# Kernel optimization log

Hardware: AMD Instinct MI355X
Metric: run time of the kernel (lower is better)

## Reference

```python
import jax, jax.numpy as jnp
import numpy as np

R, C, B, E, H = 128, 256, 1, 768, 12
DK = E // H

def setup_inputs() -> dict:
    key = jax.random.key(0)
    ks = jax.random.split(key, 5)
    s = 1.0 / np.sqrt(E)
    return {
        "x": jax.random.normal(ks[0], (R, C, B, E), jnp.float32),
        "Wq": jax.random.normal(ks[1], (E, E), jnp.float32) * s,
        "bq": jnp.zeros((E,), jnp.float32),
        "Wk": jax.random.normal(ks[2], (E, E), jnp.float32) * s,
        "bk": jnp.zeros((E,), jnp.float32),
        "Wv": jax.random.normal(ks[3], (E, E), jnp.float32) * s,
        "bv": jnp.zeros((E,), jnp.float32),
        "Wo": jax.random.normal(ks[4], (E, E), jnp.float32) * s,
        "bo": jnp.zeros((E,), jnp.float32),
    }

def reference(x, Wq, bq, Wk, bk, Wv, bv, Wo, bo):
    n_rows, n_cols, batch, emb = x.shape
    scaling = (DK ** -0.5) / jnp.sqrt(jnp.float32(n_rows))
    # projections (torch Linear: x @ W.T + b)
    q = (x @ Wq.T + bq).reshape(n_rows, n_cols, batch, H, DK) * scaling
    k = (x @ Wk.T + bk).reshape(n_rows, n_cols, batch, H, DK)
    v = (x @ Wv.T + bv).reshape(n_rows, n_cols, batch, H, DK)
    # pooled attention logits: sum over rows r -> [H, B, C, C]
    attn = jnp.einsum('rinhd,rjnhd->hnij', q, k)
    probs = jax.nn.softmax(attn, axis=-1)  # single softmax shared across rows
    # context: [R, C, B, H, DK]
    c = jnp.einsum('hnij,rjnhd->rinhd', probs, v).reshape(n_rows, n_cols, batch, emb)
    out = c @ Wo.T + bo
    return out, probs
```

## Files before the change

kernel.cpp:

```cpp
#include <hip/hip_runtime.h>
#include <math.h>

#define R_  128
#define C_  256
#define E_  768
#define H_  12
#define DK_ 64
#define T_  (R_*C_)
#define RS_ 8
#define LP  40

typedef __attribute__((ext_vector_type(8))) short          bf16x8;
typedef __attribute__((ext_vector_type(4))) float          f32x4;
typedef __attribute__((ext_vector_type(4))) unsigned short u16x4;
typedef __attribute__((ext_vector_type(8))) unsigned short u16x8;

struct HL { unsigned short h, l; };

__device__ __forceinline__ HL split2(float f) {
    HL o;
    unsigned int u = __float_as_uint(f);
    o.h = (unsigned short)(u >> 16);
    float r = f - __uint_as_float(u & 0xFFFF0000u);
    o.l = (unsigned short)(__float_as_uint(r) >> 16);
    return o;
}

template<int AMODE, int OMODE>
__global__ __launch_bounds__(256, 2) void gemm_kernel(
    const float* __restrict__ A32,
    const unsigned short* __restrict__ Ah, const unsigned short* __restrict__ Al,
    const float* __restrict__ B32, const float* __restrict__ bias, float scale,
    float* __restrict__ Y32, unsigned short* __restrict__ Yh, unsigned short* __restrict__ Yl)
{
    __shared__ __align__(16) unsigned short smem[20480];
    unsigned short* AsH = smem;
    unsigned short* AsL = smem + 5120;
    unsigned short* BsH = smem + 10240;
    unsigned short* BsL = smem + 15360;

    const int tid  = threadIdx.x;
    const int m0   = blockIdx.x * 128;
    const int n0   = blockIdx.y * 128;
    const int wave = tid >> 6, lane = tid & 63;
    const int wm   = (wave & 1) * 64, wn = (wave >> 1) * 64;
    const int fr   = lane & 15;
    const int kq   = (lane >> 4) * 8;
    const int srow = tid >> 1;
    const int sk   = (tid & 1) * 16;

    f32x4 acc[4][4] = {};

    for (int k0 = 0; k0 < E_; k0 += 32) {
        if constexpr (AMODE == 0) {
            const float* ap = A32 + (size_t)(m0 + srow) * E_ + k0 + sk;
            #pragma unroll
            for (int c = 0; c < 4; ++c) {
                float4 f = *(const float4*)(ap + 4 * c);
                u16x4 h4, l4;
                HL e0 = split2(f.x), e1 = split2(f.y), e2 = split2(f.z), e3 = split2(f.w);
                h4[0] = e0.h; h4[1] = e1.h; h4[2] = e2.h; h4[3] = e3.h;
                l4[0] = e0.l; l4[1] = e1.l; l4[2] = e2.l; l4[3] = e3.l;
                *(u16x4*)&AsH[srow * LP + sk + 4 * c] = h4;
                *(u16x4*)&AsL[srow * LP + sk + 4 * c] = l4;
            }
        } else {
            const unsigned short* aph = Ah + (size_t)(m0 + srow) * E_ + k0 + sk;
            const unsigned short* apl = Al + (size_t)(m0 + srow) * E_ + k0 + sk;
            *(u16x8*)&AsH[srow * LP + sk]     = *(const u16x8*)aph;
            *(u16x8*)&AsH[srow * LP + sk + 8] = *(const u16x8*)(aph + 8);
            *(u16x8*)&AsL[srow * LP + sk]     = *(const u16x8*)apl;
            *(u16x8*)&AsL[srow * LP + sk + 8] = *(const u16x8*)(apl + 8);
        }
        {
            const float* bp = B32 + (size_t)(n0 + srow) * E_ + k0 + sk;
            #pragma unroll
            for (int c = 0; c < 4; ++c) {
                float4 f = *(const float4*)(bp + 4 * c);
                u16x4 h4, l4;
                HL e0 = split2(f.x), e1 = split2(f.y), e2 = split2(f.z), e3 = split2(f.w);
                h4[0] = e0.h; h4[1] = e1.h; h4[2] = e2.h; h4[3] = e3.h;
                l4[0] = e0.l; l4[1] = e1.l; l4[2] = e2.l; l4[3] = e3.l;
                *(u16x4*)&BsH[srow * LP + sk + 4 * c] = h4;
                *(u16x4*)&BsL[srow * LP + sk + 4 * c] = l4;
            }
        }
        __syncthreads();

        bf16x8 a_h[4], a_l[4], b_h[4], b_l[4];
        #pragma unroll
        for (int t = 0; t < 4; ++t) {
            a_h[t] = *(const bf16x8*)&AsH[(wm + t * 16 + fr) * LP + kq];
            a_l[t] = *(const bf16x8*)&AsL[(wm + t * 16 + fr) * LP + kq];
            b_h[t] = *(const bf16x8*)&BsH[(wn + t * 16 + fr) * LP + kq];
            b_l[t] = *(const bf16x8*)&BsL[(wn + t * 16 + fr) * LP + kq];
        }
        #pragma unroll
        for (int i = 0; i < 4; ++i)
            #pragma unroll
            for (int j = 0; j < 4; ++j) {
                acc[i][j] = __builtin_amdgcn_mfma_f32_16x16x32_bf16(a_h[i], b_h[j], acc[i][j], 0, 0, 0);
                acc[i][j] = __builtin_amdgcn_mfma_f32_16x16x32_bf16(a_h[i], b_l[j], acc[i][j], 0, 0, 0);
                acc[i][j] = __builtin_amdgcn_mfma_f32_16x16x32_bf16(a_l[i], b_h[j], acc[i][j], 0, 0, 0);
            }
        __syncthreads();
    }

    float* rep = (float*)smem + wave * 1024;
    const int mr = lane >> 2;
    const int nc = (lane & 3) * 16;
    #pragma unroll
    for (int ti = 0; ti < 4; ++ti) {
        __syncthreads();
        #pragma unroll
        for (int tj = 0; tj < 4; ++tj)
            #pragma unroll
            for (int r = 0; r < 4; ++r)
                rep[((lane >> 4) * 4 + r) * 64 + tj * 16 + fr] = acc[ti][tj][r];
        __syncthreads();
        float v[16];
        #pragma unroll
        for (int c = 0; c < 4; ++c)
            *(float4*)&v[4 * c] = *(const float4*)&rep[mr * 64 + nc + 4 * c];
        const int gm = m0 + wm + ti * 16 + mr;
        const int gn = n0 + wn + nc;
        if constexpr (OMODE == 1) {
            #pragma unroll
            for (int c = 0; c < 4; ++c) {
                float4 bv = *(const float4*)&bias[gn + 4 * c];
                float4 o;
                o.x = (v[4*c+0] + bv.x) * scale; o.y = (v[4*c+1] + bv.y) * scale;
                o.z = (v[4*c+2] + bv.z) * scale; o.w = (v[4*c+3] + bv.w) * scale;
                *(float4*)&Y32[(size_t)gm * E_ + gn + 4 * c] = o;
            }
        } else {
            unsigned short hh[16], ll[16];
            #pragma unroll
            for (int c = 0; c < 4; ++c) {
                float4 bv = *(const float4*)&bias[gn + 4 * c];
                HL e0 = split2((v[4*c+0] + bv.x) * scale);
                HL e1 = split2((v[4*c+1] + bv.y) * scale);
                HL e2 = split2((v[4*c+2] + bv.z) * scale);
                HL e3 = split2((v[4*c+3] + bv.w) * scale);
                hh[4*c+0] = e0.h; ll[4*c+0] = e0.l;
                hh[4*c+1] = e1.h; ll[4*c+1] = e1.l;
                hh[4*c+2] = e2.h; ll[4*c+2] = e2.l;
                hh[4*c+3] = e3.h; ll[4*c+3] = e3.l;
            }
            u16x8 H0, H1, L0, L1;
            #pragma unroll
            for (int j = 0; j < 8; ++j) { H0[j] = hh[j]; H1[j] = hh[8+j]; L0[j] = ll[j]; L1[j] = ll[8+j]; }
            *(u16x8*)&Yh[(size_t)gm * E_ + gn]     = H0;
            *(u16x8*)&Yh[(size_t)gm * E_ + gn + 8] = H1;
            *(u16x8*)&Yl[(size_t)gm * E_ + gn]     = L0;
            *(u16x8*)&Yl[(size_t)gm * E_ + gn + 8] = L1;
        }
    }
}

__global__ __launch_bounds__(256, 2) void attn_mfma(
    const unsigned short* __restrict__ Qh, const unsigned short* __restrict__ Ql,
    const unsigned short* __restrict__ Kh, const unsigned short* __restrict__ Kl,
    float* __restrict__ part)
{
    __shared__ __align__(16) unsigned short smem[20480];
    unsigned short* AsH = smem;
    unsigned short* AsL = smem + 5120;
    unsigned short* BsH = smem + 10240;
    unsigned short* BsL = smem + 15360;

    const int tid  = threadIdx.x;
    const int i0   = blockIdx.x * 128;
    const int j0   = blockIdx.y * 128;
    const int hz   = blockIdx.z;
    const int h    = hz >> 3;
    const int rc   = hz & 7;
    const int wave = tid >> 6, lane = tid & 63;
    const int wm   = (wave & 1) * 64, wn = (wave >> 1) * 64;
    const int fr   = lane & 15;
    const int kq   = (lane >> 4) * 8;
    const int srow = tid >> 1;
    const int sk   = (tid & 1) * 16;

    f32x4 acc[4][4] = {};

    for (int s = 0; s < 32; ++s) {
        const int r  = rc * 16 + (s >> 1);
        const int d0 = (s & 1) * 32;
        const size_t qb = ((size_t)(r * C_) + i0 + srow) * E_ + h * DK_ + d0 + sk;
        const size_t kb = ((size_t)(r * C_) + j0 + srow) * E_ + h * DK_ + d0 + sk;
        *(u16x8*)&AsH[srow * LP + sk]     = *(const u16x8*)&Qh[qb];
        *(u16x8*)&AsH[srow * LP + sk + 8] = *(const u16x8*)&Qh[qb + 8];
        *(u16x8*)&AsL[srow * LP + sk]     = *(const u16x8*)&Ql[qb];
        *(u16x8*)&AsL[srow * LP + sk + 8] = *(const u16x8*)&Ql[qb + 8];
        *(u16x8*)&BsH[srow * LP + sk]     = *(const u16x8*)&Kh[kb];
        *(u16x8*)&BsH[srow * LP + sk + 8] = *(const u16x8*)&Kh[kb + 8];
        *(u16x8*)&BsL[srow * LP + sk]     = *(const u16x8*)&Kl[kb];
        *(u16x8*)&BsL[srow * LP + sk + 8] = *(const u16x8*)&Kl[kb + 8];
        __syncthreads();

        bf16x8 a_h[4], a_l[4], b_h[4], b_l[4];
        #pragma unroll
        for (int t = 0; t < 4; ++t) {
            a_h[t] = *(const bf16x8*)&AsH[(wm + t * 16 + fr) * LP + kq];
            a_l[t] = *(const bf16x8*)&AsL[(wm + t * 16 + fr) * LP + kq];
            b_h[t] = *(const bf16x8*)&BsH[(wn + t * 16 + fr) * LP + kq];
            b_l[t] = *(const bf16x8*)&BsL[(wn + t * 16 + fr) * LP + kq];
        }
        #pragma unroll
        for (int i = 0; i < 4; ++i)
            #pragma unroll
            for (int j = 0; j < 4; ++j) {
                acc[i][j] = __builtin_amdgcn_mfma_f32_16x16x32_bf16(a_h[i], b_h[j], acc[i][j], 0, 0, 0);
                acc[i][j] = __builtin_amdgcn_mfma_f32_16x16x32_bf16(a_h[i], b_l[j], acc[i][j], 0, 0, 0);
                acc[i][j] = __builtin_amdgcn_mfma_f32_16x16x32_bf16(a_l[i], b_h[j], acc[i][j], 0, 0, 0);
            }
        __syncthreads();
    }

    float* rep = (float*)smem + wave * 1024;
    const int mr = lane >> 2;
    const int nc = (lane & 3) * 16;
    #pragma unroll
    for (int ti = 0; ti < 4; ++ti) {
        __syncthreads();
        #pragma unroll
        for (int tj = 0; tj < 4; ++tj)
            #pragma unroll
            for (int r = 0; r < 4; ++r)
                rep[((lane >> 4) * 4 + r) * 64 + tj * 16 + fr] = acc[ti][tj][r];
        __syncthreads();
        const int gi = i0 + wm + ti * 16 + mr;
        const int gj = j0 + wn + nc;
        #pragma unroll
        for (int c = 0; c < 4; ++c) {
            float4 o = *(const float4*)&rep[mr * 64 + nc + 4 * c];
            *(float4*)&part[((size_t)(rc * H_ + h) * C_ + gi) * C_ + gj + 4 * c] = o;
        }
    }
}

__global__ __launch_bounds__(256) void softmax_split(
    const float* __restrict__ part, float* __restrict__ probs,
    unsigned short* __restrict__ ph, unsigned short* __restrict__ pl)
{
    const int row = blockIdx.x;
    const int j = threadIdx.x;
    const int wave = j >> 6, lane = j & 63;

    float s = 0.0f;
    #pragma unroll
    for (int rcn = 0; rcn < RS_; ++rcn)
        s += part[((size_t)rcn * H_ * C_ + row) * C_ + j];

    float m = s;
    #pragma unroll
    for (int off = 32; off > 0; off >>= 1)
        m = fmaxf(m, __shfl_down(m, off, 64));
    __shared__ float redm[4];
    if (lane == 0) redm[wave] = m;
    __syncthreads();
    m = fmaxf(fmaxf(redm[0], redm[1]), fmaxf(redm[2], redm[3]));

    float e = expf(s - m);
    float t = e;
    #pragma unroll
    for (int off = 32; off > 0; off >>= 1)
        t += __shfl_down(t, off, 64);
    __shared__ float reds[4];
    if (lane == 0) reds[wave] = t;
    __syncthreads();
    t = reds[0] + reds[1] + reds[2] + reds[3];

    float p = e / t;
    probs[(size_t)row * C_ + j] = p;
    HL sp = split2(p);
    ph[(size_t)row * C_ + j] = sp.h;
    pl[(size_t)row * C_ + j] = sp.l;
}

__global__ __launch_bounds__(256, 2) void ctx_mfma(
    const unsigned short* __restrict__ Ph, const unsigned short* __restrict__ Pl,
    const unsigned short* __restrict__ Vh, const unsigned short* __restrict__ Vl,
    unsigned short* __restrict__ Ch, unsigned short* __restrict__ Cl)
{
    __shared__ __align__(16) unsigned short smem[15360];
    unsigned short* PsH = smem;
    unsigned short* PsL = smem + 5120;
    unsigned short* VsH = smem + 10240;
    unsigned short* VsL = smem + 12800;

    const int tid  = threadIdx.x;
    const int i0   = blockIdx.x * 128;
    const int r    = blockIdx.y;
    const int h    = blockIdx.z;
    const int wave = tid >> 6, lane = tid & 63;
    const int wm   = (wave & 1) * 64, wn = (wave >> 1) * 32;
    const int fr   = lane & 15;
    const int kq   = (lane >> 4) * 8;
    const int srow = tid >> 1;
    const int sk   = (tid & 1) * 16;
    const int vjj  = tid & 31;
    const int vdg  = tid >> 5;

    f32x4 acc[4][2] = {};

    for (int s = 0; s < 8; ++s) {
        const int jb = s * 32;
        const size_t pb = ((size_t)(h * C_) + i0 + srow) * C_ + jb + sk;
        *(u16x8*)&PsH[srow * LP + sk]     = *(const u16x8*)&Ph[pb];
        *(u16x8*)&PsH[srow * LP + sk + 8] = *(const u16x8*)&Ph[pb + 8];
        *(u16x8*)&PsL[srow * LP + sk]     = *(const u16x8*)&Pl[pb];
        *(u16x8*)&PsL[srow * LP + sk + 8] = *(const u16x8*)&Pl[pb + 8];
        const size_t vb = ((size_t)(r * C_) + jb + vjj) * E_ + h * DK_ + vdg * 8;
        u16x8 v_h = *(const u16x8*)&Vh[vb];
        u16x8 v_l = *(const u16x8*)&Vl[vb];
        #pragma unroll
        for (int u = 0; u < 8; ++u) {
            VsH[(vdg * 8 + u) * LP + vjj] = v_h[u];
            VsL[(vdg * 8 + u) * LP + vjj] = v_l[u];
        }
        __syncthreads();

        bf16x8 p_h[4], p_l[4], w_h[2], w_l[2];
        #pragma unroll
        for (int t = 0; t < 4; ++t) {
            p_h[t] = *(const bf16x8*)&PsH[(wm + t * 16 + fr) * LP + kq];
            p_l[t] = *(const bf16x8*)&PsL[(wm + t * 16 + fr) * LP + kq];
        }
        #pragma unroll
        for (int t = 0; t < 2; ++t) {
            w_h[t] = *(const bf16x8*)&VsH[(wn + t * 16 + fr) * LP + kq];
            w_l[t] = *(const bf16x8*)&VsL[(wn + t * 16 + fr) * LP + kq];
        }
        #pragma unroll
        for (int i = 0; i < 4; ++i)
            #pragma unroll
            for (int j = 0; j < 2; ++j) {
                acc[i][j] = __builtin_amdgcn_mfma_f32_16x16x32_bf16(p_h[i], w_h[j], acc[i][j], 0, 0, 0);
                acc[i][j] = __builtin_amdgcn_mfma_f32_16x16x32_bf16(p_h[i], w_l[j], acc[i][j], 0, 0, 0);
                acc[i][j] = __builtin_amdgcn_mfma_f32_16x16x32_bf16(p_l[i], w_h[j], acc[i][j], 0, 0, 0);
            }
        __syncthreads();
    }

    float* rep = (float*)smem + wave * 512;
    const int mr = lane >> 2;
    const int nc = (lane & 3) * 8;
    #pragma unroll
    for (int ti = 0; ti < 4; ++ti) {
        __syncthreads();
        #pragma unroll
        for (int tj = 0; tj < 2; ++tj)
            #pragma unroll
            for (int rr = 0; rr < 4; ++rr)
                rep[((lane >> 4) * 4 + rr) * 32 + tj * 16 + fr] = acc[ti][tj][rr];
        __syncthreads();
        float v[8];
        *(float4*)&v[0] = *(const float4*)&rep[mr * 32 + nc];
        *(float4*)&v[4] = *(const float4*)&rep[mr * 32 + nc + 4];
        const int gm = r * C_ + i0 + wm + ti * 16 + mr;
        const int gn = h * DK_ + wn + nc;
        u16x8 H8, L8;
        #pragma unroll
        for (int jj = 0; jj < 8; ++jj) { HL e = split2(v[jj]); H8[jj] = e.h; L8[jj] = e.l; }
        *(u16x8*)&Ch[(size_t)gm * E_ + gn] = H8;
        *(u16x8*)&Cl[(size_t)gm * E_ + gn] = L8;
    }
}

extern "C" void kernel_launch(void* const* d_in, const int* in_sizes, int n_in,
                              void* d_out, int out_size, void* d_ws, size_t ws_size,
                              hipStream_t stream)
{
    (void)in_sizes; (void)n_in; (void)out_size; (void)ws_size;

    const float* x  = (const float*)d_in[0];
    const float* Wq = (const float*)d_in[1];
    const float* bq = (const float*)d_in[2];
    const float* Wk = (const float*)d_in[3];
    const float* bk = (const float*)d_in[4];
    const float* Wv = (const float*)d_in[5];
    const float* bv = (const float*)d_in[6];
    const float* Wo = (const float*)d_in[7];
    const float* bo = (const float*)d_in[8];

    float* out   = (float*)d_out;
    float* probs = out + (size_t)T_ * E_;
    float* part  = out;

    const size_t QN = (size_t)T_ * E_;
    unsigned short* qh = (unsigned short*)d_ws;
    unsigned short* ql = qh + QN;
    unsigned short* kh = ql + QN;
    unsigned short* kl = kh + QN;
    unsigned short* vh = kl + QN;
    unsigned short* vl = vh + QN;
    unsigned short* ph = kh;
    unsigned short* pl = kh + (size_t)H_ * C_ * C_;
    unsigned short* ch = qh;
    unsigned short* cl = ql;

    const float scaling = 0.125f / sqrtf(128.0f);

    dim3 blk(256);
    gemm_kernel<0, 0><<<dim3(T_ / 128, E_ / 128), blk, 0, stream>>>(
        x, nullptr, nullptr, Wq, bq, scaling, nullptr, qh, ql);
    gemm_kernel<0, 0><<<dim3(T_ / 128, E_ / 128), blk, 0, stream>>>(
        x, nullptr, nullptr, Wk, bk, 1.0f, nullptr, kh, kl);
    gemm_kernel<0, 0><<<dim3(T_ / 128, E_ / 128), blk, 0, stream>>>(
        x, nullptr, nullptr, Wv, bv, 1.0f, nullptr, vh, vl);

    attn_mfma<<<dim3(C_ / 128, C_ / 128, H_ * RS_), blk, 0, stream>>>(qh, ql, kh, kl, part);
    softmax_split<<<dim3(H_ * C_), blk, 0, stream>>>(part, probs, ph, pl);
    ctx_mfma<<<dim3(C_ / 128, R_, H_), blk, 0, stream>>>(ph, pl, vh, vl, ch, cl);

    gemm_kernel<1, 1><<<dim3(T_ / 128, E_ / 128), blk, 0, stream>>>(
        nullptr, ch, cl, Wo, bo, 1.0f, out, nullptr, nullptr);
}
```

Measured before the change: 879.5 us.

## Pre-split inputs to bf16 hi/lo and stage tiles via direct global-to-LDS loads

Adds a split_kernel that converts x and each weight matrix into bf16 high/low halves once, so the projection GEMMs no longer re-split fp32 tiles in every block. The GEMM and attention kernels now load tiles with global_load_lds directly into an unpadded, XOR-swizzled LDS layout, one wave per operand array, instead of going through registers. The goal is to remove redundant conversion arithmetic and register staging. The cost is extra split passes and scratch reuse of the output and workspace buffers, which must not be overwritten too early.

```diff
diff --git a/kernel.cpp b/kernel.cpp
--- a/kernel.cpp
+++ b/kernel.cpp
@@ -26,18 +26,40 @@
     return o;
 }
 
-template<int AMODE, int OMODE>
+__device__ __forceinline__ void gload16(const void* g, void* l) {
+    __builtin_amdgcn_global_load_lds(
+        (const __attribute__((address_space(1))) unsigned int*)g,
+        (__attribute__((address_space(3))) unsigned int*)l,
+        16, 0, 0);
+}
+
+__global__ __launch_bounds__(256) void split_kernel(
+    const float* __restrict__ src,
+    unsigned short* __restrict__ h, unsigned short* __restrict__ l)
+{
+    const size_t i = ((size_t)blockIdx.x * 256 + threadIdx.x) * 8;
+    float4 f0 = *(const float4*)(src + i);
+    float4 f1 = *(const float4*)(src + i + 4);
+    float v[8] = { f0.x, f0.y, f0.z, f0.w, f1.x, f1.y, f1.z, f1.w };
+    u16x8 hh, ll;
+    #pragma unroll
+    for (int j = 0; j < 8; ++j) { HL e = split2(v[j]); hh[j] = e.h; ll[j] = e.l; }
+    *(u16x8*)(h + i) = hh;
+    *(u16x8*)(l + i) = ll;
+}
+
+template<int OMODE>
 __global__ __launch_bounds__(256, 2) void gemm_kernel(
-    const float* __restrict__ A32,
     const unsigned short* __restrict__ Ah, const unsigned short* __restrict__ Al,
-    const float* __restrict__ B32, const float* __restrict__ bias, float scale,
+    const unsigned short* __restrict__ Bh, const unsigned short* __restrict__ Bl,
+    const float* __restrict__ bias, float scale,
     float* __restrict__ Y32, unsigned short* __restrict__ Yh, unsigned short* __restrict__ Yl)
 {
-    __shared__ __align__(16) unsigned short smem[20480];
-    unsigned short* AsH = smem;
-    unsigned short* AsL = smem + 5120;
-    unsigned short* BsH = smem + 10240;
-    unsigned short* BsL = smem + 15360;
+    __shared__ __align__(16) unsigned short smem[16384];
+    const unsigned short* AsH = smem;
+    const unsigned short* AsL = smem + 4096;
+    const unsigned short* BsH = smem + 8192;
+    const unsigned short* BsL = smem + 12288;
 
     const int tid  = threadIdx.x;
     const int m0   = blockIdx.x * 128;
@@ -45,55 +67,31 @@
     const int wave = tid >> 6, lane = tid & 63;
     const int wm   = (wave & 1) * 64, wn = (wave >> 1) * 64;
     const int fr   = lane & 15;
-    const int kq   = (lane >> 4) * 8;
-    const int srow = tid >> 1;
-    const int sk   = (tid & 1) * 16;
+    const int kqs  = (((lane >> 4) ^ ((fr >> 1) & 3)) * 8);
+
+    const int lrow = lane >> 2;
+    const int gd   = (lane & 3) ^ ((lane >> 3) & 3);
+    const unsigned short* gsrc = (wave == 0) ? Ah : (wave == 1) ? Al
+                               : (wave == 2) ? Bh : Bl;
+    const int rbase = (wave < 2) ? m0 : n0;
+    unsigned short* lt = smem + wave * 4096;
+    const unsigned short* sp = gsrc + (size_t)(rbase + lrow) * E_ + 8 * gd;
 
     f32x4 acc[4][4] = {};
 
     for (int k0 = 0; k0 < E_; k0 += 32) {
-        if constexpr (AMODE == 0) {
-            const float* ap = A32 + (size_t)(m0 + srow) * E_ + k0 + sk;
-            #pragma unroll
-            for (int c = 0; c < 4; ++c) {
-                float4 f = *(const float4*)(ap + 4 * c);
-                u16x4 h4, l4;
-                HL e0 = split2(f.x), e1 = split2(f.y), e2 = split2(f.z), e3 = split2(f.w);
-                h4[0] = e0.h; h4[1] = e1.h; h4[2] = e2.h; h4[3] = e3.h;
-                l4[0] = e0.l; l4[1] = e1.l; l4[2] = e2.l; l4[3] = e3.l;
-                *(u16x4*)&AsH[srow * LP + sk + 4 * c] = h4;
-                *(u16x4*)&AsL[srow * LP + sk + 4 * c] = l4;
-            }
-        } else {
-            const unsigned short* aph = Ah + (size_t)(m0 + srow) * E_ + k0 + sk;
-            const unsigned short* apl = Al + (size_t)(m0 + srow) * E_ + k0 + sk;
-            *(u16x8*)&AsH[srow * LP + sk]     = *(const u16x8*)aph;
-            *(u16x8*)&AsH[srow * LP + sk + 8] = *(const u16x8*)(aph + 8);
-            *(u16x8*)&AsL[srow * LP + sk]     = *(const u16x8*)apl;
-            *(u16x8*)&AsL[srow * LP + sk + 8] = *(const u16x8*)(apl + 8);
-        }
-        {
-            const float* bp = B32 + (size_t)(n0 + srow) * E_ + k0 + sk;
-            #pragma unroll
-            for (int c = 0; c < 4; ++c) {
-                float4 f = *(const float4*)(bp + 4 * c);
-                u16x4 h4, l4;
-                HL e0 = split2(f.x), e1 = split2(f.y), e2 = split2(f.z), e3 = split2(f.w);
-                h4[0] = e0.h; h4[1] = e1.h; h4[2] = e2.h; h4[3] = e3.h;
-                l4[0] = e0.l; l4[1] = e1.l; l4[2] = e2.l; l4[3] = e3.l;
-                *(u16x4*)&BsH[srow * LP + sk + 4 * c] = h4;
-                *(u16x4*)&BsL[srow * LP + sk + 4 * c] = l4;
-            }
-        }
+        #pragma unroll
+        for (int i = 0; i < 8; ++i)
+            gload16(sp + k0 + (size_t)i * 16 * E_, lt + i * 512);
         __syncthreads();
 
         bf16x8 a_h[4], a_l[4], b_h[4], b_l[4];
         #pragma unroll
         for (int t = 0; t < 4; ++t) {
-            a_h[t] = *(const bf16x8*)&AsH[(wm + t * 16 + fr) * LP + kq];
-            a_l[t] = *(const bf16x8*)&AsL[(wm + t * 16 + fr) * LP + kq];
-            b_h[t] = *(const bf16x8*)&BsH[(wn + t * 16 + fr) * LP + kq];
-            b_l[t] = *(const bf16x8*)&BsL[(wn + t * 16 + fr) * LP + kq];
+            a_h[t] = *(const bf16x8*)&AsH[(wm + t * 16 + fr) * 32 + kqs];
+            a_l[t] = *(const bf16x8*)&AsL[(wm + t * 16 + fr) * 32 + kqs];
+            b_h[t] = *(const bf16x8*)&BsH[(wn + t * 16 + fr) * 32 + kqs];
+            b_l[t] = *(const bf16x8*)&BsL[(wn + t * 16 + fr) * 32 + kqs];
         }
         #pragma unroll
         for (int i = 0; i < 4; ++i)
@@ -163,11 +161,11 @@
     const unsigned short* __restrict__ Kh, const unsigned short* __restrict__ Kl,
     float* __restrict__ part)
 {
-    __shared__ __align__(16) unsigned short smem[20480];
-    unsigned short* AsH = smem;
-    unsigned short* AsL = smem + 5120;
-    unsigned short* BsH = smem + 10240;
-    unsigned short* BsL = smem + 15360;
+    __shared__ __align__(16) unsigned short smem[16384];
+    const unsigned short* AsH = smem;
+    const unsigned short* AsL = smem + 4096;
+    const unsigned short* BsH = smem + 8192;
+    const unsigned short* BsL = smem + 12288;
 
     const int tid  = threadIdx.x;
     const int i0   = blockIdx.x * 128;
@@ -178,34 +176,34 @@
     const int wave = tid >> 6, lane = tid & 63;
     const int wm   = (wave & 1) * 64, wn = (wave >> 1) * 64;
     const int fr   = lane & 15;
-    const int kq   = (lane >> 4) * 8;
-    const int srow = tid >> 1;
-    const int sk   = (tid & 1) * 16;
+    const int kqs  = (((lane >> 4) ^ ((fr >> 1) & 3)) * 8);
+
+    const int lrow = lane >> 2;
+    const int gd   = (lane & 3) ^ ((lane >> 3) & 3);
+    const unsigned short* gsrc = (wave == 0) ? Qh : (wave == 1) ? Ql
+                               : (wave == 2) ? Kh : Kl;
+    const int rbase = (wave < 2) ? i0 : j0;
+    unsigned short* lt = smem + wave * 4096;
 
     f32x4 acc[4][4] = {};
 
     for (int s = 0; s < 32; ++s) {
         const int r  = rc * 16 + (s >> 1);
         const int d0 = (s & 1) * 32;
-        const size_t qb = ((size_t)(r * C_) + i0 + srow) * E_ + h * DK_ + d0 + sk;
-        const size_t kb = ((size_t)(r * C_) + j0 + srow) * E_ + h * DK_ + d0 + sk;
-        *(u16x8*)&AsH[srow * LP + sk]     = *(const u16x8*)&Qh[qb];
-        *(u16x8*)&AsH[srow * LP + sk + 8] = *(const u16x8*)&Qh[qb + 8];
-        *(u16x8*)&AsL[srow * LP + sk]     = *(const u16x8*)&Ql[qb];
-        *(u16x8*)&AsL[srow * LP + sk + 8] = *(const u16x8*)&Ql[qb + 8];
-        *(u16x8*)&BsH[srow * LP + sk]     = *(const u16x8*)&Kh[kb];
-        *(u16x8*)&BsH[srow * LP + sk + 8] = *(const u16x8*)&Kh[kb + 8];
-        *(u16x8*)&BsL[srow * LP + sk]     = *(const u16x8*)&Kl[kb];
-        *(u16x8*)&BsL[srow * LP + sk + 8] = *(const u16x8*)&Kl[kb + 8];
+        const unsigned short* sp =
+            gsrc + ((size_t)(r * C_) + rbase + lrow) * E_ + h * DK_ + d0 + 8 * gd;
+        #pragma unroll
+        for (int i = 0; i < 8; ++i)
+            gload16(sp + (size_t)i * 16 * E_, lt + i * 512);
         __syncthreads();
 
         bf16x8 a_h[4], a_l[4], b_h[4], b_l[4];
         #pragma unroll
         for (int t = 0; t < 4; ++t) {
-            a_h[t] = *(const bf16x8*)&AsH[(wm + t * 16 + fr) * LP + kq];
-            a_l[t] = *(const bf16x8*)&AsL[(wm + t * 16 + fr) * LP + kq];
-            b_h[t] = *(const bf16x8*)&BsH[(wn + t * 16 + fr) * LP + kq];
-            b_l[t] = *(const bf16x8*)&BsL[(wn + t * 16 + fr) * LP + kq];
+            a_h[t] = *(const bf16x8*)&AsH[(wm + t * 16 + fr) * 32 + kqs];
+            a_l[t] = *(const bf16x8*)&AsL[(wm + t * 16 + fr) * 32 + kqs];
+            b_h[t] = *(const bf16x8*)&BsH[(wn + t * 16 + fr) * 32 + kqs];
+            b_l[t] = *(const bf16x8*)&BsL[(wn + t * 16 + fr) * 32 + kqs];
         }
         #pragma unroll
         for (int i = 0; i < 4; ++i)
@@ -390,6 +388,7 @@
     float* part  = out;
 
     const size_t QN = (size_t)T_ * E_;
+    const size_t WN = (size_t)E_ * E_;
     unsigned short* qh = (unsigned short*)d_ws;
     unsigned short* ql = qh + QN;
     unsigned short* kh = ql + QN;
@@ -401,20 +400,40 @@
     unsigned short* ch = qh;
     unsigned short* cl = ql;
 
+    unsigned short* xh   = (unsigned short*)out;
+    unsigned short* xl   = xh + QN;
+    unsigned short* wsph = (unsigned short*)probs;
+    unsigned short* wspl = wsph + WN;
+    unsigned short* woh  = kl;
+    unsigned short* wol  = kl + WN;
+
     const float scaling = 0.125f / sqrtf(128.0f);
 
     dim3 blk(256);
-    gemm_kernel<0, 0><<<dim3(T_ / 128, E_ / 128), blk, 0, stream>>>(
-        x, nullptr, nullptr, Wq, bq, scaling, nullptr, qh, ql);
-    gemm_kernel<0, 0><<<dim3(T_ / 128, E_ / 128), blk, 0, stream>>>(
-        x, nullptr, nullptr, Wk, bk, 1.0f, nullptr, kh, kl);
-    gemm_kernel<0, 0><<<dim3(T_ / 128, E_ / 128), blk, 0, stream>>>(
-        x, nullptr, nullptr, Wv, bv, 1.0f, nullptr, vh, vl);
+    const int xblocks = (int)(QN / 2048);
+    const int wblocks = (int)(WN / 2048);
+
+    split_kernel<<<dim3(xblocks), blk, 0, stream>>>(x, xh, xl);
+
+    split_kernel<<<dim3(wblocks), blk, 0, stream>>>(Wq, wsph, wspl);
+    gemm_kernel<0><<<dim3(T_ / 128, E_ / 128), blk, 0, stream>>>(
+        xh, xl, wsph, wspl, bq, scaling, nullptr, qh, ql);
+
+    split_kernel<<<dim3(wblocks), blk, 0, stream>>>(Wk, wsph, wspl);
+    gemm_kernel<0><<<dim3(T_ / 128, E_ / 128), blk, 0, stream>>>(
+        xh, xl, wsph, wspl, bk, 1.0f, nullptr, kh, kl);
+
+    split_kernel<<<dim3(wblocks), blk, 0, stream>>>(Wv, wsph, wspl);
+    gemm_kernel<0><<<dim3(T_ / 128, E_ / 128), blk, 0, stream>>>(
+        xh, xl, wsph, wspl, bv, 1.0f, nullptr, vh, vl);
 
     attn_mfma<<<dim3(C_ / 128, C_ / 128, H_ * RS_), blk, 0, stream>>>(qh, ql, kh, kl, part);
+
+    split_kernel<<<dim3(wblocks), blk, 0, stream>>>(Wo, woh, wol);
+
     softmax_split<<<dim3(H_ * C_), blk, 0, stream>>>(part, probs, ph, pl);
     ctx_mfma<<<dim3(C_ / 128, R_, H_), blk, 0, stream>>>(ph, pl, vh, vl, ch, cl);
 
-    gemm_kernel<1, 1><<<dim3(T_ / 128, E_ / 128), blk, 0, stream>>>(
-        nullptr, ch, cl, Wo, bo, 1.0f, out, nullptr, nullptr);
-}
+    gemm_kernel<1><<<dim3(T_ / 128, E_ / 128), blk, 0, stream>>>(
+        ch, cl, woh, wol, bo, 1.0f, out, nullptr, nullptr);
+}
```

Measured after the change: 915.3 us. 4.1% more time.
